# Optimization experiments

Hardware: AMD Instinct MI355X
Metric: run time of the kernel (lower is better)

The kernel has to match this reference:

```python
import jax, jax.numpy as jnp
import numpy as np

B, T, D, H = 8, 2048, 1024, 16
HD = D // H          # head_dim = 64
SC = H               # scales = n_heads = 16
DECAY_MIN, DECAY_MAX = 0.3, 0.99


def setup_inputs() -> dict:
    key = jax.random.key(0)
    k_x, k_in, k_mix, k_gw, k_gb, k_out = jax.random.split(key, 6)
    x = jax.random.normal(k_x, (B, T, D), dtype=jnp.float32)
    pad_mask = jnp.zeros((B, T), dtype=bool)  # True = PAD
    inv = 1.0 / np.sqrt(D)
    W_in = jax.random.uniform(k_in, (D, D), jnp.float32, -inv, inv)
    W_out = jax.random.uniform(k_out, (D, D), jnp.float32, -inv, inv)
    W_gate = jax.random.uniform(k_gw, (D, D), jnp.float32, -inv, inv)
    b_gate = jax.random.uniform(k_gb, (D,), jnp.float32, -inv, inv)
    state_mix = jax.random.normal(k_mix, (H, SC, HD), jnp.float32) / np.sqrt(HD)
    p = jnp.linspace(DECAY_MIN, DECAY_MAX, SC)
    logit_decay = jnp.tile(jnp.log(p / (1.0 - p))[None, :], (H, 1))  # [H, SC]
    return {"x": x, "pad_mask": pad_mask, "W_in": W_in, "state_mix": state_mix,
            "logit_decay": logit_decay, "W_gate": W_gate, "b_gate": b_gate,
            "W_out": W_out}


def reference(x, pad_mask, W_in, state_mix, logit_decay, W_gate, b_gate, W_out):
    Bc, Tc, Dc = x.shape
    Hc, Sc, Hd = state_mix.shape
    h = (x @ W_in.T).reshape(Bc, Tc, Hc, Hd)          # [B,T,H,Hd]
    decays = jax.nn.sigmoid(logit_decay)              # [H,SC]
    keep = 1.0 - pad_mask.astype(x.dtype)             # [B,T], 1 where not PAD

    def step(S, inp):
        ht, mt = inp                                  # [B,H,Hd], [B]
        S = (decays[None, :, :, None] * S + ht[:, :, None, :]) \
            * mt[:, None, None, None]                 # [B,H,SC,Hd]
        read = jnp.einsum('bhsd,hsd->bhd', S, state_mix)
        return S, read

    S0 = jnp.zeros((Bc, Hc, Sc, Hd), dtype=x.dtype)
    _, reads = jax.lax.scan(step, S0, (h.transpose(1, 0, 2, 3), keep.T))
    y = reads.transpose(1, 0, 2, 3).reshape(Bc, Tc, Dc)
    g = jax.nn.sigmoid(x @ W_gate.T + b_gate)
    y = g * y + (1.0 - g) * x
    return y @ W_out.T
```

## Files before the change

### kernel.cpp

```cpp
#include <hip/hip_runtime.h>

#define B_  8
#define T_  2048
#define D_  1024
#define H_  16
#define HD_ 64
#define SC_ 16
#define NC_ 32
#define CT_ 64

typedef __attribute__((ext_vector_type(8))) short short8;
typedef __attribute__((ext_vector_type(4))) float f32x4;

__device__ inline unsigned short f2bf(float f) {
  union { float f; unsigned u; } v; v.f = f;
  unsigned r = v.u + 0x7FFFu + ((v.u >> 16) & 1u);
  return (unsigned short)(r >> 16);
}
__device__ inline float bf2f(unsigned short b) {
  union { unsigned u; float f; } v; v.u = ((unsigned)b) << 16; return v.f;
}

__device__ inline void gl_lds16(const unsigned short* g, unsigned short* l) {
  __builtin_amdgcn_global_load_lds(
      (const __attribute__((address_space(1))) unsigned int*)(g),
      (__attribute__((address_space(3))) unsigned int*)(l), 16, 0, 0);
}

__global__ void conv_f32_bf16(const float* __restrict__ in,
                              unsigned short* __restrict__ out, int n4) {
  int i = blockIdx.x * 256 + threadIdx.x;
  if (i >= n4) return;
  float4 v = ((const float4*)in)[i];
  ushort4 o;
  o.x = f2bf(v.x); o.y = f2bf(v.y); o.z = f2bf(v.z); o.w = f2bf(v.w);
  ((ushort4*)out)[i] = o;
}

template<int OUT_BF16>
__global__ __launch_bounds__(256, 2)
void gemm_bt(const unsigned short* __restrict__ A,
             const unsigned short* __restrict__ Bt,
             void* __restrict__ Cout, int M, int N, int K) {
  __shared__ unsigned short As[128 * 64];
  __shared__ unsigned short Bs[128 * 64];
  const int tid  = threadIdx.x;
  const int lane = tid & 63;
  const int w    = tid >> 6;
  const int wm   = w >> 1, wn = w & 1;
  const int l15  = lane & 15, l4 = lane >> 4;
  const int srow   = lane >> 3;
  const int schunk = (lane & 7) ^ srow;
  const int nbn  = N >> 7;
  const int nwg  = gridDim.x;
  int bid = blockIdx.x;
  int b2 = ((nwg & 7) == 0) ? ((bid & 7) * (nwg >> 3) + (bid >> 3)) : bid;
  const int bm = (b2 / nbn) << 7;
  const int bn = (b2 % nbn) << 7;

  f32x4 acc[4][4] = {};

  for (int k0 = 0; k0 < K; k0 += 64) {
#pragma unroll
    for (int i = 0; i < 4; ++i) {
      int q = (w << 2) + i;
      int r = (q << 3) + srow;
      gl_lds16(A  + (size_t)(bm + r) * K + k0 + (schunk << 3), As + (q << 9));
      gl_lds16(Bt + (size_t)(bn + r) * K + k0 + (schunk << 3), Bs + (q << 9));
    }
    __syncthreads();
#pragma unroll
    for (int ks = 0; ks < 2; ++ks) {
      short8 af[4], bf[4];
#pragma unroll
      for (int i = 0; i < 4; ++i) {
        int ra = (wm << 6) + (i << 4) + l15;
        int kc = (ks << 2) + l4;
        af[i] = *(const short8*)(&As[ra * 64 + ((kc ^ (ra & 7)) << 3)]);
        int rb = (wn << 6) + (i << 4) + l15;
        bf[i] = *(const short8*)(&Bs[rb * 64 + ((kc ^ (rb & 7)) << 3)]);
      }
#pragma unroll
      for (int mi = 0; mi < 4; ++mi)
#pragma unroll
        for (int ni = 0; ni < 4; ++ni)
          acc[mi][ni] = __builtin_amdgcn_mfma_f32_16x16x32_bf16(
              af[mi], bf[ni], acc[mi][ni], 0, 0, 0);
    }
    __syncthreads();
  }

  const int rbase = bm + (wm << 6) + (l4 << 2);
  const int cbase = bn + (wn << 6) + l15;
#pragma unroll
  for (int mi = 0; mi < 4; ++mi)
#pragma unroll
    for (int ni = 0; ni < 4; ++ni)
#pragma unroll
      for (int r = 0; r < 4; ++r) {
        size_t row = rbase + (mi << 4) + r;
        int col = cbase + (ni << 4);
        if (OUT_BF16)
          ((unsigned short*)Cout)[row * N + col] = f2bf(acc[mi][ni][r]);
        else
          ((float*)Cout)[row * N + col] = acc[mi][ni][r];
      }
}

__global__ void scan_pass1(const unsigned short* __restrict__ hb,
                           const unsigned char* __restrict__ pad,
                           const float* __restrict__ ldec,
                           float* __restrict__ Schunk,
                           float* __restrict__ akeep) {
  int gid = blockIdx.x * 256 + threadIdx.x;
  int d  = gid & 63;
  int hh = (gid >> 6) & 15;
  int c  = (gid >> 10) & (NC_ - 1);
  int b  = gid >> 15;
  float dec[SC_], S[SC_];
#pragma unroll
  for (int s = 0; s < SC_; ++s) {
    dec[s] = 1.f / (1.f + __expf(-ldec[hh * SC_ + s]));
    S[s] = 0.f;
  }
  const int t0 = c * CT_;
  const unsigned short* hp = hb + (size_t)(b * T_ + t0) * D_ + hh * HD_ + d;
  const unsigned char* pp = pad + b * T_ + t0;
  float ak = 1.f;
  for (int t = 0; t < CT_; ++t) {
    float ht = bf2f(*hp); hp += D_;
    float k = pp[t] ? 0.f : 1.f;
    ak = fminf(ak, k);
#pragma unroll
    for (int s = 0; s < SC_; ++s) S[s] = (dec[s] * S[s] + ht) * k;
  }
  size_t base = ((size_t)((b * NC_ + c) * H_ + hh) * SC_) * HD_ + d;
#pragma unroll
  for (int s = 0; s < SC_; ++s) Schunk[base + s * HD_] = S[s];
  if (hh == 0 && d == 0) akeep[b * NC_ + c] = ak;
}

__global__ void scan_combine(float* __restrict__ Schunk,
                             const float* __restrict__ akeep,
                             const float* __restrict__ ldec) {
  int gid = blockIdx.x * 256 + threadIdx.x;
  int d  = gid & 63;
  int s  = (gid >> 6) & 15;
  int hh = (gid >> 10) & 15;
  int b  = gid >> 14;
  float dec  = 1.f / (1.f + __expf(-ldec[hh * SC_ + s]));
  float dpow = __powf(dec, (float)CT_);
  float carry = 0.f;
  for (int c = 0; c < NC_; ++c) {
    size_t idx = ((size_t)((b * NC_ + c) * H_ + hh) * SC_ + s) * HD_ + d;
    float e = Schunk[idx];
    Schunk[idx] = carry;
    float Ac = (akeep[b * NC_ + c] != 0.f) ? dpow : 0.f;
    carry = Ac * carry + e;
  }
}

__global__ void scan_pass2(const unsigned short* __restrict__ hb,
                           const unsigned char* __restrict__ pad,
                           const float* __restrict__ ldec,
                           const float* __restrict__ mix,
                           const float* __restrict__ Sstart,
                           const unsigned short* __restrict__ gpre,
                           const float* __restrict__ bgate,
                           unsigned short* __restrict__ xy) {
  int gid = blockIdx.x * 256 + threadIdx.x;
  int d  = gid & 63;
  int hh = (gid >> 6) & 15;
  int c  = (gid >> 10) & (NC_ - 1);
  int b  = gid >> 15;
  float dec[SC_], mx[SC_], S[SC_];
  size_t sbase = ((size_t)((b * NC_ + c) * H_ + hh) * SC_) * HD_ + d;
#pragma unroll
  for (int s = 0; s < SC_; ++s) {
    dec[s] = 1.f / (1.f + __expf(-ldec[hh * SC_ + s]));
    mx[s]  = mix[(hh * SC_ + s) * HD_ + d];
    S[s]   = Sstart[sbase + s * HD_];
  }
  const int t0 = c * CT_;
  const int col = hh * HD_ + d;
  const float bg = bgate[col];
  size_t off = (size_t)(b * T_ + t0) * D_ + col;
  const unsigned char* pp = pad + b * T_ + t0;
  for (int t = 0; t < CT_; ++t, off += D_) {
    float ht = bf2f(hb[off]);
    float k = pp[t] ? 0.f : 1.f;
    float rd = 0.f;
#pragma unroll
    for (int s = 0; s < SC_; ++s) {
      S[s] = (dec[s] * S[s] + ht) * k;
      rd += mx[s] * S[s];
    }
    float g  = 1.f / (1.f + __expf(-(bf2f(gpre[off]) + bg)));
    float xv = bf2f(xy[off]);
    xy[off] = f2bf(g * rd + (1.f - g) * xv);
  }
}

extern "C" void kernel_launch(void* const* d_in, const int* in_sizes, int n_in,
                              void* d_out, int out_size, void* d_ws, size_t ws_size,
                              hipStream_t stream) {
  const float* x          = (const float*)d_in[0];
  const unsigned char* pm = (const unsigned char*)d_in[1];
  const float* W_in       = (const float*)d_in[2];
  const float* smix       = (const float*)d_in[3];
  const float* ldec       = (const float*)d_in[4];
  const float* W_gate     = (const float*)d_in[5];
  const float* b_gate     = (const float*)d_in[6];
  const float* W_out      = (const float*)d_in[7];
  float* out = (float*)d_out;
  char* ws = (char*)d_ws;

  const int NX = B_ * T_ * D_;
  const int NW = D_ * D_;

  unsigned short* xb    = (unsigned short*)(ws);
  unsigned short* wbin  = (unsigned short*)(ws + 33554432);
  unsigned short* wbgt  = (unsigned short*)(ws + 35651584);
  unsigned short* wbout = (unsigned short*)(ws + 37748736);
  unsigned short* hb    = (unsigned short*)(ws + 39845888);
  float* Schunk         = (float*)(ws + 73400320);
  float* akeep          = (float*)(ws + 90177536);
  unsigned short* gpre  = (unsigned short*)d_out;

  conv_f32_bf16<<<NX / 1024, 256, 0, stream>>>(x, xb, NX / 4);
  conv_f32_bf16<<<NW / 1024, 256, 0, stream>>>(W_in,   wbin,  NW / 4);
  conv_f32_bf16<<<NW / 1024, 256, 0, stream>>>(W_gate, wbgt,  NW / 4);
  conv_f32_bf16<<<NW / 1024, 256, 0, stream>>>(W_out,  wbout, NW / 4);

  const int M = B_ * T_;
  dim3 gg((M / 128) * (D_ / 128));

  gemm_bt<1><<<gg, 256, 0, stream>>>(xb, wbin, hb,   M, D_, D_);
  gemm_bt<1><<<gg, 256, 0, stream>>>(xb, wbgt, gpre, M, D_, D_);

  dim3 sg1(B_ * NC_ * H_ * HD_ / 256);
  dim3 sgc(B_ * H_ * SC_ * HD_ / 256);
  scan_pass1 <<<sg1, 256, 0, stream>>>(hb, pm, ldec, Schunk, akeep);
  scan_combine<<<sgc, 256, 0, stream>>>(Schunk, akeep, ldec);
  scan_pass2 <<<sg1, 256, 0, stream>>>(hb, pm, ldec, smix, Schunk, gpre, b_gate, xb);

  gemm_bt<0><<<gg, 256, 0, stream>>>(xb, wbout, out, M, D_, D_);
}
```

Baseline: 215.6 us.

## Fuse input and gate GEMMs and vectorize the chunked scan over pairs

The input and gate projections become one N=2048 GEMM. It relies on the bf16 W_in and W_gate copies sitting next to each other in the workspace, and each output tile is routed to either hb or gpre. The scan kernels now process two head-dim elements per thread with packed bf16 loads and stores. The pad mask is precomputed as a bitmask so padded steps take a branch instead of a multiply. The chunk size changes from 64 to 32 steps, which doubles the number of chunks and makes the serial combine loop longer. Schunk moves into the unused upper half of the output buffer. The goal is to cut launch count, re-reads of x, and scan memory-instruction overhead, at the cost of fewer threads in the combine pass.

After: 259.5 us. 20.3% more time.

```diff
diff --git a/kernel.cpp b/kernel.cpp
--- a/kernel.cpp
+++ b/kernel.cpp
@@ -6,11 +6,12 @@
 #define H_  16
 #define HD_ 64
 #define SC_ 16
-#define NC_ 32
-#define CT_ 64
+#define NC_ 64
+#define CT_ 32
 
 typedef __attribute__((ext_vector_type(8))) short short8;
 typedef __attribute__((ext_vector_type(4))) float f32x4;
+typedef __attribute__((ext_vector_type(2))) float f32x2;
 
 __device__ inline unsigned short f2bf(float f) {
   union { float f; unsigned u; } v; v.f = f;
@@ -19,6 +20,14 @@
 }
 __device__ inline float bf2f(unsigned short b) {
   union { unsigned u; float f; } v; v.u = ((unsigned)b) << 16; return v.f;
+}
+__device__ inline f32x2 bfp2f(unsigned u) {
+  union { unsigned u; float f; } a, b;
+  a.u = u << 16; b.u = u & 0xFFFF0000u;
+  f32x2 r; r.x = a.f; r.y = b.f; return r;
+}
+__device__ inline unsigned f2bfp(f32x2 v) {
+  return ((unsigned)f2bf(v.x)) | (((unsigned)f2bf(v.y)) << 16);
 }
 
 __device__ inline void gl_lds16(const unsigned short* g, unsigned short* l) {
@@ -37,11 +46,12 @@
   ((ushort4*)out)[i] = o;
 }
 
-template<int OUT_BF16>
+template<int MODE>
 __global__ __launch_bounds__(256, 2)
 void gemm_bt(const unsigned short* __restrict__ A,
              const unsigned short* __restrict__ Bt,
-             void* __restrict__ Cout, int M, int N, int K) {
+             void* __restrict__ C1, void* __restrict__ C2,
+             int M, int N, int K) {
   __shared__ unsigned short As[128 * 64];
   __shared__ unsigned short Bs[128 * 64];
   const int tid  = threadIdx.x;
@@ -91,7 +101,11 @@
   }
 
   const int rbase = bm + (wm << 6) + (l4 << 2);
-  const int cbase = bn + (wn << 6) + l15;
+  void* dst = C1;
+  int cb = bn;
+  if (MODE == 2 && bn >= 1024) { dst = C2; cb = bn - 1024; }
+  const int cbase = cb + (wn << 6) + l15;
+  const int CN = (MODE == 2) ? 1024 : N;
 #pragma unroll
   for (int mi = 0; mi < 4; ++mi)
 #pragma unroll
@@ -100,10 +114,10 @@
       for (int r = 0; r < 4; ++r) {
         size_t row = rbase + (mi << 4) + r;
         int col = cbase + (ni << 4);
-        if (OUT_BF16)
-          ((unsigned short*)Cout)[row * N + col] = f2bf(acc[mi][ni][r]);
+        if (MODE == 0)
+          ((float*)dst)[row * CN + col] = acc[mi][ni][r];
         else
-          ((float*)Cout)[row * N + col] = acc[mi][ni][r];
+          ((unsigned short*)dst)[row * CN + col] = f2bf(acc[mi][ni][r]);
       }
 }
 
@@ -113,48 +127,54 @@
                            float* __restrict__ Schunk,
                            float* __restrict__ akeep) {
   int gid = blockIdx.x * 256 + threadIdx.x;
-  int d  = gid & 63;
-  int hh = (gid >> 6) & 15;
-  int c  = (gid >> 10) & (NC_ - 1);
+  int d2 = gid & 31;
+  int hh = (gid >> 5) & 15;
+  int c  = (gid >> 9) & (NC_ - 1);
   int b  = gid >> 15;
-  float dec[SC_], S[SC_];
+  float dec[SC_];
+  f32x2 S[SC_];
 #pragma unroll
   for (int s = 0; s < SC_; ++s) {
     dec[s] = 1.f / (1.f + __expf(-ldec[hh * SC_ + s]));
-    S[s] = 0.f;
+    S[s].x = 0.f; S[s].y = 0.f;
   }
   const int t0 = c * CT_;
-  const unsigned short* hp = hb + (size_t)(b * T_ + t0) * D_ + hh * HD_ + d;
+  const unsigned short* hp = hb + (size_t)(b * T_ + t0) * D_ + hh * HD_ + d2 * 2;
   const unsigned char* pp = pad + b * T_ + t0;
-  float ak = 1.f;
+  unsigned pmask = 0;
+#pragma unroll
+  for (int t = 0; t < CT_; ++t) pmask |= (pp[t] ? 1u : 0u) << t;
   for (int t = 0; t < CT_; ++t) {
-    float ht = bf2f(*hp); hp += D_;
-    float k = pp[t] ? 0.f : 1.f;
-    ak = fminf(ak, k);
-#pragma unroll
-    for (int s = 0; s < SC_; ++s) S[s] = (dec[s] * S[s] + ht) * k;
-  }
-  size_t base = ((size_t)((b * NC_ + c) * H_ + hh) * SC_) * HD_ + d;
-#pragma unroll
-  for (int s = 0; s < SC_; ++s) Schunk[base + s * HD_] = S[s];
-  if (hh == 0 && d == 0) akeep[b * NC_ + c] = ak;
+    f32x2 h2 = bfp2f(*(const unsigned*)hp); hp += D_;
+    if ((pmask >> t) & 1u) {
+#pragma unroll
+      for (int s = 0; s < SC_; ++s) { S[s].x = 0.f; S[s].y = 0.f; }
+    } else {
+#pragma unroll
+      for (int s = 0; s < SC_; ++s) S[s] = dec[s] * S[s] + h2;
+    }
+  }
+  size_t base = ((size_t)((b * NC_ + c) * H_ + hh) * SC_) * HD_ + d2 * 2;
+#pragma unroll
+  for (int s = 0; s < SC_; ++s) *(f32x2*)(&Schunk[base + s * HD_]) = S[s];
+  if (hh == 0 && d2 == 0) akeep[b * NC_ + c] = pmask ? 0.f : 1.f;
 }
 
 __global__ void scan_combine(float* __restrict__ Schunk,
                              const float* __restrict__ akeep,
                              const float* __restrict__ ldec) {
   int gid = blockIdx.x * 256 + threadIdx.x;
-  int d  = gid & 63;
-  int s  = (gid >> 6) & 15;
-  int hh = (gid >> 10) & 15;
-  int b  = gid >> 14;
+  int d2 = gid & 31;
+  int s  = (gid >> 5) & 15;
+  int hh = (gid >> 9) & 15;
+  int b  = gid >> 13;
   float dec  = 1.f / (1.f + __expf(-ldec[hh * SC_ + s]));
   float dpow = __powf(dec, (float)CT_);
-  float carry = 0.f;
+  f32x2 carry; carry.x = 0.f; carry.y = 0.f;
   for (int c = 0; c < NC_; ++c) {
-    size_t idx = ((size_t)((b * NC_ + c) * H_ + hh) * SC_ + s) * HD_ + d;
-    float e = Schunk[idx];
-    Schunk[idx] = carry;
+    size_t idx = ((size_t)((b * NC_ + c) * H_ + hh) * SC_ + s) * HD_ + d2 * 2;
+    f32x2 e = *(f32x2*)(&Schunk[idx]);
+    *(f32x2*)(&Schunk[idx]) = carry;
     float Ac = (akeep[b * NC_ + c] != 0.f) ? dpow : 0.f;
     carry = Ac * carry + e;
   }
@@ -169,35 +189,47 @@
                            const float* __restrict__ bgate,
                            unsigned short* __restrict__ xy) {
   int gid = blockIdx.x * 256 + threadIdx.x;
-  int d  = gid & 63;
-  int hh = (gid >> 6) & 15;
-  int c  = (gid >> 10) & (NC_ - 1);
+  int d2 = gid & 31;
+  int hh = (gid >> 5) & 15;
+  int c  = (gid >> 9) & (NC_ - 1);
   int b  = gid >> 15;
-  float dec[SC_], mx[SC_], S[SC_];
-  size_t sbase = ((size_t)((b * NC_ + c) * H_ + hh) * SC_) * HD_ + d;
+  float dec[SC_];
+  f32x2 mx[SC_], S[SC_];
+  size_t sbase = ((size_t)((b * NC_ + c) * H_ + hh) * SC_) * HD_ + d2 * 2;
 #pragma unroll
   for (int s = 0; s < SC_; ++s) {
     dec[s] = 1.f / (1.f + __expf(-ldec[hh * SC_ + s]));
-    mx[s]  = mix[(hh * SC_ + s) * HD_ + d];
-    S[s]   = Sstart[sbase + s * HD_];
+    mx[s] = *(const f32x2*)(&mix[(hh * SC_ + s) * HD_ + d2 * 2]);
+    S[s]  = *(const f32x2*)(&Sstart[sbase + s * HD_]);
   }
   const int t0 = c * CT_;
-  const int col = hh * HD_ + d;
-  const float bg = bgate[col];
+  const int col = hh * HD_ + d2 * 2;
+  f32x2 bg = *(const f32x2*)(&bgate[col]);
   size_t off = (size_t)(b * T_ + t0) * D_ + col;
   const unsigned char* pp = pad + b * T_ + t0;
+  unsigned pmask = 0;
+#pragma unroll
+  for (int t = 0; t < CT_; ++t) pmask |= (pp[t] ? 1u : 0u) << t;
   for (int t = 0; t < CT_; ++t, off += D_) {
-    float ht = bf2f(hb[off]);
-    float k = pp[t] ? 0.f : 1.f;
-    float rd = 0.f;
-#pragma unroll
-    for (int s = 0; s < SC_; ++s) {
-      S[s] = (dec[s] * S[s] + ht) * k;
-      rd += mx[s] * S[s];
-    }
-    float g  = 1.f / (1.f + __expf(-(bf2f(gpre[off]) + bg)));
-    float xv = bf2f(xy[off]);
-    xy[off] = f2bf(g * rd + (1.f - g) * xv);
+    f32x2 h2 = bfp2f(*(const unsigned*)(hb + off));
+    f32x2 rd; rd.x = 0.f; rd.y = 0.f;
+    if ((pmask >> t) & 1u) {
+#pragma unroll
+      for (int s = 0; s < SC_; ++s) { S[s].x = 0.f; S[s].y = 0.f; }
+    } else {
+#pragma unroll
+      for (int s = 0; s < SC_; ++s) {
+        S[s] = dec[s] * S[s] + h2;
+        rd  += mx[s] * S[s];
+      }
+    }
+    f32x2 gp = bfp2f(*(const unsigned*)(gpre + off));
+    f32x2 g;
+    g.x = 1.f / (1.f + __expf(-(gp.x + bg.x)));
+    g.y = 1.f / (1.f + __expf(-(gp.y + bg.y)));
+    f32x2 xv = bfp2f(*(const unsigned*)(xy + off));
+    f32x2 y = g * rd + (1.f - g) * xv;
+    *(unsigned*)(xy + off) = f2bfp(y);
   }
 }
 
@@ -223,9 +255,9 @@
   unsigned short* wbgt  = (unsigned short*)(ws + 35651584);
   unsigned short* wbout = (unsigned short*)(ws + 37748736);
   unsigned short* hb    = (unsigned short*)(ws + 39845888);
-  float* Schunk         = (float*)(ws + 73400320);
-  float* akeep          = (float*)(ws + 90177536);
+  float* akeep          = (float*)(ws + 73400320);
   unsigned short* gpre  = (unsigned short*)d_out;
+  float* Schunk         = (float*)((char*)d_out + 33554432);
 
   conv_f32_bf16<<<NX / 1024, 256, 0, stream>>>(x, xb, NX / 4);
   conv_f32_bf16<<<NW / 1024, 256, 0, stream>>>(W_in,   wbin,  NW / 4);
@@ -233,16 +265,16 @@
   conv_f32_bf16<<<NW / 1024, 256, 0, stream>>>(W_out,  wbout, NW / 4);
 
   const int M = B_ * T_;
-  dim3 gg((M / 128) * (D_ / 128));
-
-  gemm_bt<1><<<gg, 256, 0, stream>>>(xb, wbin, hb,   M, D_, D_);
-  gemm_bt<1><<<gg, 256, 0, stream>>>(xb, wbgt, gpre, M, D_, D_);
-
-  dim3 sg1(B_ * NC_ * H_ * HD_ / 256);
-  dim3 sgc(B_ * H_ * SC_ * HD_ / 256);
+
+  dim3 gg2((M / 128) * (2048 / 128));
+  gemm_bt<2><<<gg2, 256, 0, stream>>>(xb, wbin, hb, gpre, M, 2048, D_);
+
+  dim3 sg1(B_ * NC_ * H_ * (HD_ / 2) / 256);
+  dim3 sgc(B_ * H_ * SC_ * (HD_ / 2) / 256);
   scan_pass1 <<<sg1, 256, 0, stream>>>(hb, pm, ldec, Schunk, akeep);
   scan_combine<<<sgc, 256, 0, stream>>>(Schunk, akeep, ldec);
   scan_pass2 <<<sg1, 256, 0, stream>>>(hb, pm, ldec, smix, Schunk, gpre, b_gate, xb);
 
-  gemm_bt<0><<<gg, 256, 0, stream>>>(xb, wbout, out, M, D_, D_);
-}
+  dim3 gg((M / 128) * (D_ / 128));
+  gemm_bt<0><<<gg, 256, 0, stream>>>(xb, wbout, out, nullptr, M, D_, D_);
+}
```

## Fuse input and gate GEMMs, apply gate sigmoid in epilogue, add pad-free scan path

Applied to the files above, without the earlier changes.

Runs the W_in and W_gate projections as one GEMM over a concatenated 2048-wide weight. This relies on the two bf16 weight buffers sitting next to each other in the workspace. The epilogue routes the gate half to a separate buffer and applies bias plus sigmoid there, so scan_pass2 no longer computes the exponential. Both scan passes check once per chunk whether any pad is present and, if none is, run a branch-free recurrence without the keep multiply. The goal is to cut one launch, reuse the x tile across both weight sets, and remove per-step mask work; the cost is extra epilogue logic and a dependence on the workspace layout.

After: 197.2 us. 8.5% less time.

```diff
diff --git a/kernel.cpp b/kernel.cpp
--- a/kernel.cpp
+++ b/kernel.cpp
@@ -37,11 +37,13 @@
   ((ushort4*)out)[i] = o;
 }
 
-template<int OUT_BF16>
+template<int MODE>
 __global__ __launch_bounds__(256, 2)
 void gemm_bt(const unsigned short* __restrict__ A,
              const unsigned short* __restrict__ Bt,
-             void* __restrict__ Cout, int M, int N, int K) {
+             void* __restrict__ C1, void* __restrict__ C2,
+             const float* __restrict__ bgate,
+             int M, int N, int K) {
   __shared__ unsigned short As[128 * 64];
   __shared__ unsigned short Bs[128 * 64];
   const int tid  = threadIdx.x;
@@ -91,7 +93,16 @@
   }
 
   const int rbase = bm + (wm << 6) + (l4 << 2);
-  const int cbase = bn + (wn << 6) + l15;
+  const bool is_gate = (MODE == 2) && (bn >= 1024);
+  void* dst = is_gate ? C2 : C1;
+  const int cb = is_gate ? (bn - 1024) : bn;
+  const int cbase = cb + (wn << 6) + l15;
+  const int CN = (MODE == 2) ? 1024 : N;
+  float bgv[4];
+  if (is_gate) {
+#pragma unroll
+    for (int ni = 0; ni < 4; ++ni) bgv[ni] = bgate[cbase + (ni << 4)];
+  }
 #pragma unroll
   for (int mi = 0; mi < 4; ++mi)
 #pragma unroll
@@ -100,11 +111,23 @@
       for (int r = 0; r < 4; ++r) {
         size_t row = rbase + (mi << 4) + r;
         int col = cbase + (ni << 4);
-        if (OUT_BF16)
-          ((unsigned short*)Cout)[row * N + col] = f2bf(acc[mi][ni][r]);
-        else
-          ((float*)Cout)[row * N + col] = acc[mi][ni][r];
-      }
+        if (MODE == 0) {
+          ((float*)dst)[row * CN + col] = acc[mi][ni][r];
+        } else if (is_gate) {
+          float g = 1.f / (1.f + __expf(-(acc[mi][ni][r] + bgv[ni])));
+          ((unsigned short*)dst)[row * CN + col] = f2bf(g);
+        } else {
+          ((unsigned short*)dst)[row * CN + col] = f2bf(acc[mi][ni][r]);
+        }
+      }
+}
+
+__device__ inline bool chunk_has_pad(const unsigned char* pp) {
+  const unsigned long long* p8 = (const unsigned long long*)pp;
+  unsigned long long v = 0;
+#pragma unroll
+  for (int i = 0; i < CT_ / 8; ++i) v |= p8[i];
+  return v != 0ull;
 }
 
 __global__ void scan_pass1(const unsigned short* __restrict__ hb,
@@ -126,18 +149,25 @@
   const int t0 = c * CT_;
   const unsigned short* hp = hb + (size_t)(b * T_ + t0) * D_ + hh * HD_ + d;
   const unsigned char* pp = pad + b * T_ + t0;
-  float ak = 1.f;
-  for (int t = 0; t < CT_; ++t) {
-    float ht = bf2f(*hp); hp += D_;
-    float k = pp[t] ? 0.f : 1.f;
-    ak = fminf(ak, k);
-#pragma unroll
-    for (int s = 0; s < SC_; ++s) S[s] = (dec[s] * S[s] + ht) * k;
+  bool anypad = chunk_has_pad(pp);
+  if (!anypad) {
+    for (int t = 0; t < CT_; ++t) {
+      float ht = bf2f(*hp); hp += D_;
+#pragma unroll
+      for (int s = 0; s < SC_; ++s) S[s] = dec[s] * S[s] + ht;
+    }
+  } else {
+    for (int t = 0; t < CT_; ++t) {
+      float ht = bf2f(*hp); hp += D_;
+      float k = pp[t] ? 0.f : 1.f;
+#pragma unroll
+      for (int s = 0; s < SC_; ++s) S[s] = (dec[s] * S[s] + ht) * k;
+    }
   }
   size_t base = ((size_t)((b * NC_ + c) * H_ + hh) * SC_) * HD_ + d;
 #pragma unroll
   for (int s = 0; s < SC_; ++s) Schunk[base + s * HD_] = S[s];
-  if (hh == 0 && d == 0) akeep[b * NC_ + c] = ak;
+  if (hh == 0 && d == 0) akeep[b * NC_ + c] = anypad ? 0.f : 1.f;
 }
 
 __global__ void scan_combine(float* __restrict__ Schunk,
@@ -165,8 +195,7 @@
                            const float* __restrict__ ldec,
                            const float* __restrict__ mix,
                            const float* __restrict__ Sstart,
-                           const unsigned short* __restrict__ gpre,
-                           const float* __restrict__ bgate,
+                           const unsigned short* __restrict__ gb,
                            unsigned short* __restrict__ xy) {
   int gid = blockIdx.x * 256 + threadIdx.x;
   int d  = gid & 63;
@@ -183,21 +212,36 @@
   }
   const int t0 = c * CT_;
   const int col = hh * HD_ + d;
-  const float bg = bgate[col];
   size_t off = (size_t)(b * T_ + t0) * D_ + col;
   const unsigned char* pp = pad + b * T_ + t0;
-  for (int t = 0; t < CT_; ++t, off += D_) {
-    float ht = bf2f(hb[off]);
-    float k = pp[t] ? 0.f : 1.f;
-    float rd = 0.f;
-#pragma unroll
-    for (int s = 0; s < SC_; ++s) {
-      S[s] = (dec[s] * S[s] + ht) * k;
-      rd += mx[s] * S[s];
-    }
-    float g  = 1.f / (1.f + __expf(-(bf2f(gpre[off]) + bg)));
-    float xv = bf2f(xy[off]);
-    xy[off] = f2bf(g * rd + (1.f - g) * xv);
+  bool anypad = chunk_has_pad(pp);
+  if (!anypad) {
+    for (int t = 0; t < CT_; ++t, off += D_) {
+      float ht = bf2f(hb[off]);
+      float rd = 0.f;
+#pragma unroll
+      for (int s = 0; s < SC_; ++s) {
+        S[s] = dec[s] * S[s] + ht;
+        rd  += mx[s] * S[s];
+      }
+      float g  = bf2f(gb[off]);
+      float xv = bf2f(xy[off]);
+      xy[off] = f2bf(fmaf(g, rd - xv, xv));
+    }
+  } else {
+    for (int t = 0; t < CT_; ++t, off += D_) {
+      float ht = bf2f(hb[off]);
+      float k = pp[t] ? 0.f : 1.f;
+      float rd = 0.f;
+#pragma unroll
+      for (int s = 0; s < SC_; ++s) {
+        S[s] = (dec[s] * S[s] + ht) * k;
+        rd  += mx[s] * S[s];
+      }
+      float g  = bf2f(gb[off]);
+      float xv = bf2f(xy[off]);
+      xy[off] = f2bf(fmaf(g, rd - xv, xv));
+    }
   }
 }
 
@@ -225,7 +269,7 @@
   unsigned short* hb    = (unsigned short*)(ws + 39845888);
   float* Schunk         = (float*)(ws + 73400320);
   float* akeep          = (float*)(ws + 90177536);
-  unsigned short* gpre  = (unsigned short*)d_out;
+  unsigned short* gb    = (unsigned short*)d_out;
 
   conv_f32_bf16<<<NX / 1024, 256, 0, stream>>>(x, xb, NX / 4);
   conv_f32_bf16<<<NW / 1024, 256, 0, stream>>>(W_in,   wbin,  NW / 4);
@@ -233,16 +277,16 @@
   conv_f32_bf16<<<NW / 1024, 256, 0, stream>>>(W_out,  wbout, NW / 4);
 
   const int M = B_ * T_;
-  dim3 gg((M / 128) * (D_ / 128));
-
-  gemm_bt<1><<<gg, 256, 0, stream>>>(xb, wbin, hb,   M, D_, D_);
-  gemm_bt<1><<<gg, 256, 0, stream>>>(xb, wbgt, gpre, M, D_, D_);
+
+  dim3 gg2((M / 128) * (2048 / 128));
+  gemm_bt<2><<<gg2, 256, 0, stream>>>(xb, wbin, hb, gb, b_gate, M, 2048, D_);
 
   dim3 sg1(B_ * NC_ * H_ * HD_ / 256);
   dim3 sgc(B_ * H_ * SC_ * HD_ / 256);
   scan_pass1 <<<sg1, 256, 0, stream>>>(hb, pm, ldec, Schunk, akeep);
   scan_combine<<<sgc, 256, 0, stream>>>(Schunk, akeep, ldec);
-  scan_pass2 <<<sg1, 256, 0, stream>>>(hb, pm, ldec, smix, Schunk, gpre, b_gate, xb);
-
-  gemm_bt<0><<<gg, 256, 0, stream>>>(xb, wbout, out, M, D_, D_);
-}
+  scan_pass2 <<<sg1, 256, 0, stream>>>(hb, pm, ldec, smix, Schunk, gb, xb);
+
+  dim3 gg((M / 128) * (D_ / 128));
+  gemm_bt<0><<<gg, 256, 0, stream>>>(xb, wbout, out, nullptr, nullptr, M, D_, D_);
+}
```
